# Optimization experiments

Measured on AMD Instinct MI355X. Metric: run time of the kernel, lower is better.

## Reference

```python
import jax, jax.numpy as jnp
import numpy as np

K_NEIGHBOURS = 40  # includes self; self is dropped after top-k


def setup_inputs() -> dict:
    key = jax.random.key(0)
    ks = jax.random.split(key, 4)
    B, V, F_in = 4, 4096, 64
    P, S, F_out = 64, 4, 64
    x = jax.random.normal(ks[0], (B, V, F_in), dtype=jnp.float32)
    Wf = jax.random.normal(ks[1], (F_in, P), dtype=jnp.float32) / np.sqrt(F_in)
    bf = jnp.zeros((P,), dtype=jnp.float32)
    Ws = jax.random.normal(ks[2], (F_in, S), dtype=jnp.float32) / np.sqrt(F_in)
    bs = jnp.zeros((S,), dtype=jnp.float32)
    Wo = jax.random.normal(ks[3], (F_in + 2 * P, F_out), dtype=jnp.float32) / np.sqrt(F_in + 2 * P)
    bo = jnpp = jnp.zeros((F_out,), dtype=jnp.float32)
    return {"x": x, "Wf": Wf, "bf": bf, "Ws": Ws, "bs": bs, "Wo": Wo, "bo": bo}


def _euclidean_squared(c):
    # c: [B, V, S] -> [B, V, V] squared pairwise distances
    sq = jnp.sum(c * c, axis=-1)  # [B, V]
    d2 = sq[:, :, None] + sq[:, None, :] - 2.0 * jnp.einsum('bvs,bus->bvu', c, c)
    return d2


def reference(x, Wf, bf, Ws, bs, Wo, bo):
    # learned spatial coordinates and propagated features
    coords = x @ Ws + bs            # [B, V, S]
    feats = x @ Wf + bf             # [B, V, P]

    d2 = _euclidean_squared(coords)                 # [B, V, V]
    neg_vals, idx = jax.lax.top_k(-d2, K_NEIGHBOURS)  # closest first (self at 0)
    nbr_idx = idx[:, :, 1:]                         # [B, V, K-1]
    dist = -neg_vals[:, :, 1:]                      # [B, V, K-1] (>= 0)

    # gauss_of_lin(d * 10) = exp(-|10 d|)
    w = jnp.exp(-jnp.abs(dist * 10.0))              # [B, V, K-1]

    # gather neighbour features per batch: [B, V, K-1, P]
    nf = jax.vmap(lambda f, i: f[i])(feats, nbr_idx)
    nf = nf * w[..., None]

    collected = jnp.concatenate([jnp.max(nf, axis=2), jnp.mean(nf, axis=2)], axis=-1)  # [B, V, 2P]
    updated = jnp.concatenate([x, collected], axis=-1)  # [B, V, F_in + 2P]
    return jnp.tanh(updated @ Wo + bo)
```

## Files before the change

### kernel.cpp

```cpp
#include <hip/hip_runtime.h>
#include <cmath>

#define BB  4
#define VV  4096
#define KK  40
#define FIN 64

typedef float v2f __attribute__((ext_vector_type(2)));

__global__ __launch_bounds__(256) void prep_kernel(
    const float* __restrict__ x, const float* __restrict__ Wf,
    const float* __restrict__ bf, const float* __restrict__ Ws,
    const float* __restrict__ bs,
    float* __restrict__ coords, float* __restrict__ sq,
    float* __restrict__ feats)
{
    int lane = threadIdx.x & 63;
    int wid  = threadIdx.x >> 6;
    int row0 = (blockIdx.x * 4 + wid) * 4;
    const float* xr = x + (size_t)row0 * FIN;

    float rx0 = xr[lane];
    float rx1 = xr[64  + lane];
    float rx2 = xr[128 + lane];
    float rx3 = xr[192 + lane];

    float a0 = 0.f, a1 = 0.f, a2 = 0.f, a3 = 0.f;
    #pragma unroll
    for (int k = 0; k < FIN; ++k) {
        float wf = Wf[k * 64 + lane];
        a0 = fmaf(__uint_as_float(
             __builtin_amdgcn_readlane(__float_as_uint(rx0), k)), wf, a0);
        a1 = fmaf(__uint_as_float(
             __builtin_amdgcn_readlane(__float_as_uint(rx1), k)), wf, a1);
        a2 = fmaf(__uint_as_float(
             __builtin_amdgcn_readlane(__float_as_uint(rx2), k)), wf, a2);
        a3 = fmaf(__uint_as_float(
             __builtin_amdgcn_readlane(__float_as_uint(rx3), k)), wf, a3);
    }
    float bfl = bf[lane];
    feats[(size_t)(row0 + 0) * 64 + lane] = a0 + bfl;
    feats[(size_t)(row0 + 1) * 64 + lane] = a1 + bfl;
    feats[(size_t)(row0 + 2) * 64 + lane] = a2 + bfl;
    feats[(size_t)(row0 + 3) * 64 + lane] = a3 + bfl;

    int r  = lane >> 4;
    int s  = (lane >> 2) & 3;
    int kc = lane & 3;
    const float* xrr = x + (size_t)(row0 + r) * FIN + kc * 16;
    const float* wsr = Ws + kc * 16 * 4 + s;
    float c = 0.f;
    #pragma unroll
    for (int k = 0; k < 16; ++k)
        c = fmaf(xrr[k], wsr[k * 4], c);
    c += __shfl_xor(c, 1, 64);
    c += __shfl_xor(c, 2, 64);
    float val = c + bs[s];
    if ((lane & 3) == 0) coords[(size_t)(row0 + r) * 4 + s] = val;
    float p = val * val;
    p += __shfl_xor(p, 4, 64);
    p += __shfl_xor(p, 8, 64);
    if ((lane & 15) == 0) sq[row0 + r] = p;
}

__device__ __forceinline__ unsigned umed3(unsigned a, unsigned b, unsigned c)
{
    unsigned d;
    asm("v_med3_u32 %0, %1, %2, %3" : "=v"(d) : "v"(a), "v"(b), "v"(c));
    return d;
}

__device__ __forceinline__ unsigned bfi_key(unsigned maskv, unsigned d2b,
                                            unsigned u)
{
    unsigned d;
    asm("v_bfi_b32 %0, %1, %2, %3" : "=v"(d) : "v"(maskv), "v"(d2b), "v"(u));
    return d;
}

__device__ __forceinline__ int cnt_lt4(unsigned m0, unsigned m1,
                                       unsigned m2, unsigned m3,
                                       unsigned cand)
{
    return (int)__popcll(__ballot(m0 < cand))
         + (int)__popcll(__ballot(m1 < cand))
         + (int)__popcll(__ballot(m2 < cand))
         + (int)__popcll(__ballot(m3 < cand));
}

__device__ __forceinline__ unsigned select_thresh(unsigned m0, unsigned m1,
                                                  unsigned m2, unsigned m3)
{
    unsigned M = 0u;
    #pragma unroll
    for (int bit = 30; bit >= 12; --bit) {
        unsigned cand = M | (1u << bit);
        if (cnt_lt4(m0, m1, m2, m3, cand) <= 39) M = cand;
    }
    unsigned Msel = M | 0xFFFu;
    if (cnt_lt4(m0, m1, m2, m3, M + 4096u) != 40) {
        #pragma unroll
        for (int bit = 11; bit >= 0; --bit) {
            unsigned cand = M | (1u << bit);
            if (cnt_lt4(m0, m1, m2, m3, cand) <= 39) M = cand;
        }
        Msel = M;
    }
    return Msel;
}

__device__ __forceinline__ void compact4(unsigned m0, unsigned m1,
                                         unsigned m2, unsigned m3,
                                         unsigned Msel, uint2* dst)
{
    unsigned mn = m0;
    #pragma unroll
    for (int off = 32; off >= 1; off >>= 1) {
        unsigned o = __shfl_xor(mn, off, 64);
        mn = o < mn ? o : mn;
    }
    int base = 0;
    unsigned kk = m0;
    #pragma unroll
    for (int i = 0; i < 4; ++i) {
        bool pred = (kk <= Msel) && (kk != mn);
        unsigned long long mask = __ballot(pred);
        unsigned pos = (unsigned)base +
            __builtin_amdgcn_mbcnt_hi((unsigned)(mask >> 32),
                __builtin_amdgcn_mbcnt_lo((unsigned)mask, 0u));
        if (pred) {
            float d2a = __uint_as_float(kk & 0xFFFFF000u);
            float w   = __expf(-10.f * d2a);
            dst[pos] = make_uint2((kk & 4095u) << 8, __float_as_uint(w));
        }
        base += (int)__popcll(mask);
        kk = (i == 0) ? m1 : (i == 1) ? m2 : m3;
    }
}

__global__ __launch_bounds__(128, 8) void gravnet_kernel(
    const float* __restrict__ x, const float* __restrict__ coords,
    const float* __restrict__ sq, const float* __restrict__ feats,
    const float* __restrict__ Wo, const float* __restrict__ bo,
    float* __restrict__ out)
{
    int lane = threadIdx.x & 63;
    int w    = threadIdx.x >> 6;
    int bid  = (int)((blockIdx.x & 7) * 512 + (blockIdx.x >> 3));
    int gw   = bid * 2 + w;
    int qb   = gw * 2;
    int b    = qb >> 12;
    int v0   = qb & (VV - 1);

    __shared__ __align__(16) char smem[4096];
    uint2* s_nb  = (uint2*)(smem + w * 2048);
    float* s_upd = (float*)(smem + w * 2048);

    const float4* cb  = (const float4*)(coords + (size_t)b * VV * 4);
    const float*  sqb = sq + (size_t)b * VV;

    float4 cq0 = cb[v0], cq1 = cb[v0 + 1];
    v2f nxA = (v2f){-2.f * cq0.x, -2.f * cq1.x};
    v2f nyA = (v2f){-2.f * cq0.y, -2.f * cq1.y};
    v2f nzA = (v2f){-2.f * cq0.z, -2.f * cq1.z};
    v2f nwA = (v2f){-2.f * cq0.w, -2.f * cq1.w};
    v2f hsA = (v2f){sqb[v0], sqb[v0 + 1]};

    unsigned k00 = ~0u, k01 = ~0u, k02 = ~0u, k03 = ~0u;
    unsigned k10 = ~0u, k11 = ~0u, k12 = ~0u, k13 = ~0u;

    unsigned maskv = 0xFFFFF000u;

    #pragma unroll 8
    for (int i = 0; i < 64; ++i) {
        int u = i * 64 + lane;
        float4 cu = cb[u];
        float squ = sqb[u];
        v2f accA = hsA + (v2f){squ, squ};
        accA = __builtin_elementwise_fma(nxA, (v2f){cu.x, cu.x}, accA);
        accA = __builtin_elementwise_fma(nyA, (v2f){cu.y, cu.y}, accA);
        accA = __builtin_elementwise_fma(nzA, (v2f){cu.z, cu.z}, accA);
        accA = __builtin_elementwise_fma(nwA, (v2f){cu.w, cu.w}, accA);

        {
            float d2 = fmaxf(accA.x, 0.f);
            unsigned k = bfi_key(maskv, __float_as_uint(d2), (unsigned)u);
            unsigned n1 = umed3(k00, k01, k);
            unsigned n2 = umed3(k01, k02, k);
            unsigned n3 = umed3(k02, k03, k);
            k00 = min(k00, k); k01 = n1; k02 = n2; k03 = n3;
        }
        {
            float d2 = fmaxf(accA.y, 0.f);
            unsigned k = bfi_key(maskv, __float_as_uint(d2), (unsigned)u);
            unsigned n1 = umed3(k10, k11, k);
            unsigned n2 = umed3(k11, k12, k);
            unsigned n3 = umed3(k12, k13, k);
            k10 = min(k10, k); k11 = n1; k12 = n2; k13 = n3;
        }
    }

    compact4(k00, k01, k02, k03,
             select_thresh(k00, k01, k02, k03), &s_nb[0]);
    compact4(k10, k11, k12, k13,
             select_thresh(k10, k11, k12, k13), &s_nb[KK]);

    const float* fb  = feats + (size_t)b * VV * 64;
    const char*  fbl = (const char*)(fb + lane);
    const uint4* nb0 = (const uint4*)&s_nb[0];
    const uint4* nb1 = (const uint4*)&s_nb[KK];
    v2f vmax01 = (v2f){-INFINITY, -INFINITY};
    v2f vsum01 = (v2f){0.f, 0.f};
    #pragma unroll 4
    for (int jp = 0; jp < 19; ++jp) {
        uint4 a = nb0[jp];
        uint4 c = nb1[jp];
        float f0a = *(const float*)(fbl + a.x);
        float f1a = *(const float*)(fbl + c.x);
        float f0b = *(const float*)(fbl + a.z);
        float f1b = *(const float*)(fbl + c.z);
        v2f ga = (v2f){f0a, f1a} *
                 (v2f){__uint_as_float(a.y), __uint_as_float(c.y)};
        v2f gb = (v2f){f0b, f1b} *
                 (v2f){__uint_as_float(a.w), __uint_as_float(c.w)};
        vmax01 = __builtin_elementwise_max(vmax01,
                 __builtin_elementwise_max(ga, gb));
        vsum01 += ga + gb;
    }
    {
        uint2 n0 = s_nb[38];
        uint2 n1 = s_nb[KK + 38];
        float f0 = *(const float*)(fbl + n0.x);
        float f1 = *(const float*)(fbl + n1.x);
        v2f g01 = (v2f){f0, f1} *
                  (v2f){__uint_as_float(n0.y), __uint_as_float(n1.y)};
        vmax01 = __builtin_elementwise_max(vmax01, g01);
        vsum01 += g01;
    }

    int q0g = qb, q1g = qb + 1;
    float* sb = s_upd;
    *(float2*)&sb[lane * 2] =
        make_float2(x[(size_t)q0g * 64 + lane], x[(size_t)q1g * 64 + lane]);
    *(float2*)&sb[128 + lane * 2] = make_float2(vmax01.x, vmax01.y);
    *(float2*)&sb[256 + lane * 2] =
        make_float2(vsum01.x * (1.0f / 39.0f), vsum01.y * (1.0f / 39.0f));

    float bol = bo[lane];
    v2f acc01 = (v2f){bol, bol};
    #pragma unroll 8
    for (int jj = 0; jj < 96; ++jj) {
        float wo0 = Wo[(jj * 2 + 0) * 64 + lane];
        float wo1 = Wo[(jj * 2 + 1) * 64 + lane];
        float4 up = *(const float4*)&sb[jj * 4];
        acc01 = __builtin_elementwise_fma((v2f){up.x, up.y},
                                          (v2f){wo0, wo0}, acc01);
        acc01 = __builtin_elementwise_fma((v2f){up.z, up.w},
                                          (v2f){wo1, wo1}, acc01);
    }
    float e0t = __expf(2.f * acc01.x);
    float e1t = __expf(2.f * acc01.y);
    out[(size_t)q0g * 64 + lane] = 1.f - __fdividef(2.f, e0t + 1.f);
    out[(size_t)q1g * 64 + lane] = 1.f - __fdividef(2.f, e1t + 1.f);
}

extern "C" void kernel_launch(void* const* d_in, const int* in_sizes, int n_in,
                              void* d_out, int out_size, void* d_ws, size_t ws_size,
                              hipStream_t stream)
{
    (void)in_sizes; (void)n_in; (void)out_size; (void)ws_size;
    const float* x  = (const float*)d_in[0];
    const float* Wf = (const float*)d_in[1];
    const float* bf = (const float*)d_in[2];
    const float* Ws = (const float*)d_in[3];
    const float* bs = (const float*)d_in[4];
    const float* Wo = (const float*)d_in[5];
    const float* bo = (const float*)d_in[6];
    float* out = (float*)d_out;

    float* coords = (float*)d_ws;
    float* sq     = coords + (size_t)BB * VV * 4;
    float* feats  = sq + (size_t)BB * VV;

    prep_kernel<<<BB * VV / 16, 256, 0, stream>>>(x, Wf, bf, Ws, bs,
                                                  coords, sq, feats);
    gravnet_kernel<<<BB * VV / 4, 128, 0, stream>>>(x, coords, sq, feats,
                                                    Wo, bo, out);
}
```

Before: 126.9 us.

## Process four queries per wave and four waves per block in gravnet kernel

Each wavefront now handles four query points instead of two. Every loaded candidate coordinate and every Wo row is reused across four queries, which halves global and L2 traffic per query for the distance scan and the output projection. Blocks grow from 128 to 256 threads with a matching grid and LDS size, and the launch bounds change to (256,4). The cost is more registers for the extra top-k state and accumulators, which may lower occupancy, and the grid has half as many waves, which reduces latency hiding.

```diff
diff --git a/kernel.cpp b/kernel.cpp
--- a/kernel.cpp
+++ b/kernel.cpp
@@ -138,7 +138,7 @@
     }
 }
 
-__global__ __launch_bounds__(128, 8) void gravnet_kernel(
+__global__ __launch_bounds__(256, 4) void gravnet_kernel(
     const float* __restrict__ x, const float* __restrict__ coords,
     const float* __restrict__ sq, const float* __restrict__ feats,
     const float* __restrict__ Wo, const float* __restrict__ bo,
@@ -146,32 +146,40 @@
 {
     int lane = threadIdx.x & 63;
     int w    = threadIdx.x >> 6;
-    int bid  = (int)((blockIdx.x & 7) * 512 + (blockIdx.x >> 3));
-    int gw   = bid * 2 + w;
-    int qb   = gw * 2;
+    int bid  = (int)((blockIdx.x & 7) * 128 + (blockIdx.x >> 3));
+    int gw   = bid * 4 + w;
+    int qb   = gw * 4;
     int b    = qb >> 12;
     int v0   = qb & (VV - 1);
 
-    __shared__ __align__(16) char smem[4096];
-    uint2* s_nb  = (uint2*)(smem + w * 2048);
-    float* s_upd = (float*)(smem + w * 2048);
+    __shared__ __align__(16) char smem[12288];
+    uint2* s_nb  = (uint2*)(smem + w * 3072);
+    float* s_upd = (float*)(smem + w * 3072);
 
     const float4* cb  = (const float4*)(coords + (size_t)b * VV * 4);
     const float*  sqb = sq + (size_t)b * VV;
 
-    float4 cq0 = cb[v0], cq1 = cb[v0 + 1];
+    float4 cq0 = cb[v0],     cq1 = cb[v0 + 1];
+    float4 cq2 = cb[v0 + 2], cq3 = cb[v0 + 3];
     v2f nxA = (v2f){-2.f * cq0.x, -2.f * cq1.x};
     v2f nyA = (v2f){-2.f * cq0.y, -2.f * cq1.y};
     v2f nzA = (v2f){-2.f * cq0.z, -2.f * cq1.z};
     v2f nwA = (v2f){-2.f * cq0.w, -2.f * cq1.w};
     v2f hsA = (v2f){sqb[v0], sqb[v0 + 1]};
+    v2f nxB = (v2f){-2.f * cq2.x, -2.f * cq3.x};
+    v2f nyB = (v2f){-2.f * cq2.y, -2.f * cq3.y};
+    v2f nzB = (v2f){-2.f * cq2.z, -2.f * cq3.z};
+    v2f nwB = (v2f){-2.f * cq2.w, -2.f * cq3.w};
+    v2f hsB = (v2f){sqb[v0 + 2], sqb[v0 + 3]};
 
     unsigned k00 = ~0u, k01 = ~0u, k02 = ~0u, k03 = ~0u;
     unsigned k10 = ~0u, k11 = ~0u, k12 = ~0u, k13 = ~0u;
+    unsigned k20 = ~0u, k21 = ~0u, k22 = ~0u, k23 = ~0u;
+    unsigned k30 = ~0u, k31 = ~0u, k32 = ~0u, k33 = ~0u;
 
     unsigned maskv = 0xFFFFF000u;
 
-    #pragma unroll 8
+    #pragma unroll 4
     for (int i = 0; i < 64; ++i) {
         int u = i * 64 + lane;
         float4 cu = cb[u];
@@ -181,6 +189,11 @@
         accA = __builtin_elementwise_fma(nyA, (v2f){cu.y, cu.y}, accA);
         accA = __builtin_elementwise_fma(nzA, (v2f){cu.z, cu.z}, accA);
         accA = __builtin_elementwise_fma(nwA, (v2f){cu.w, cu.w}, accA);
+        v2f accB = hsB + (v2f){squ, squ};
+        accB = __builtin_elementwise_fma(nxB, (v2f){cu.x, cu.x}, accB);
+        accB = __builtin_elementwise_fma(nyB, (v2f){cu.y, cu.y}, accB);
+        accB = __builtin_elementwise_fma(nzB, (v2f){cu.z, cu.z}, accB);
+        accB = __builtin_elementwise_fma(nwB, (v2f){cu.w, cu.w}, accB);
 
         {
             float d2 = fmaxf(accA.x, 0.f);
@@ -198,70 +211,122 @@
             unsigned n3 = umed3(k12, k13, k);
             k10 = min(k10, k); k11 = n1; k12 = n2; k13 = n3;
         }
+        {
+            float d2 = fmaxf(accB.x, 0.f);
+            unsigned k = bfi_key(maskv, __float_as_uint(d2), (unsigned)u);
+            unsigned n1 = umed3(k20, k21, k);
+            unsigned n2 = umed3(k21, k22, k);
+            unsigned n3 = umed3(k22, k23, k);
+            k20 = min(k20, k); k21 = n1; k22 = n2; k23 = n3;
+        }
+        {
+            float d2 = fmaxf(accB.y, 0.f);
+            unsigned k = bfi_key(maskv, __float_as_uint(d2), (unsigned)u);
+            unsigned n1 = umed3(k30, k31, k);
+            unsigned n2 = umed3(k31, k32, k);
+            unsigned n3 = umed3(k32, k33, k);
+            k30 = min(k30, k); k31 = n1; k32 = n2; k33 = n3;
+        }
     }
 
     compact4(k00, k01, k02, k03,
-             select_thresh(k00, k01, k02, k03), &s_nb[0]);
+             select_thresh(k00, k01, k02, k03), &s_nb[0 * KK]);
     compact4(k10, k11, k12, k13,
-             select_thresh(k10, k11, k12, k13), &s_nb[KK]);
+             select_thresh(k10, k11, k12, k13), &s_nb[1 * KK]);
+    compact4(k20, k21, k22, k23,
+             select_thresh(k20, k21, k22, k23), &s_nb[2 * KK]);
+    compact4(k30, k31, k32, k33,
+             select_thresh(k30, k31, k32, k33), &s_nb[3 * KK]);
 
     const float* fb  = feats + (size_t)b * VV * 64;
     const char*  fbl = (const char*)(fb + lane);
-    const uint4* nb0 = (const uint4*)&s_nb[0];
-    const uint4* nb1 = (const uint4*)&s_nb[KK];
+    const uint4* nb0 = (const uint4*)&s_nb[0 * KK];
+    const uint4* nb1 = (const uint4*)&s_nb[1 * KK];
+    const uint4* nb2 = (const uint4*)&s_nb[2 * KK];
+    const uint4* nb3 = (const uint4*)&s_nb[3 * KK];
     v2f vmax01 = (v2f){-INFINITY, -INFINITY};
     v2f vsum01 = (v2f){0.f, 0.f};
-    #pragma unroll 4
+    v2f vmax23 = (v2f){-INFINITY, -INFINITY};
+    v2f vsum23 = (v2f){0.f, 0.f};
+    #pragma unroll 2
     for (int jp = 0; jp < 19; ++jp) {
         uint4 a = nb0[jp];
         uint4 c = nb1[jp];
+        uint4 e = nb2[jp];
+        uint4 g = nb3[jp];
         float f0a = *(const float*)(fbl + a.x);
         float f1a = *(const float*)(fbl + c.x);
+        float f2a = *(const float*)(fbl + e.x);
+        float f3a = *(const float*)(fbl + g.x);
         float f0b = *(const float*)(fbl + a.z);
         float f1b = *(const float*)(fbl + c.z);
-        v2f ga = (v2f){f0a, f1a} *
-                 (v2f){__uint_as_float(a.y), __uint_as_float(c.y)};
-        v2f gb = (v2f){f0b, f1b} *
-                 (v2f){__uint_as_float(a.w), __uint_as_float(c.w)};
+        float f2b = *(const float*)(fbl + e.z);
+        float f3b = *(const float*)(fbl + g.z);
+        v2f ga01 = (v2f){f0a, f1a} *
+                   (v2f){__uint_as_float(a.y), __uint_as_float(c.y)};
+        v2f gb01 = (v2f){f0b, f1b} *
+                   (v2f){__uint_as_float(a.w), __uint_as_float(c.w)};
+        v2f ga23 = (v2f){f2a, f3a} *
+                   (v2f){__uint_as_float(e.y), __uint_as_float(g.y)};
+        v2f gb23 = (v2f){f2b, f3b} *
+                   (v2f){__uint_as_float(e.w), __uint_as_float(g.w)};
         vmax01 = __builtin_elementwise_max(vmax01,
-                 __builtin_elementwise_max(ga, gb));
-        vsum01 += ga + gb;
+                 __builtin_elementwise_max(ga01, gb01));
+        vsum01 += ga01 + gb01;
+        vmax23 = __builtin_elementwise_max(vmax23,
+                 __builtin_elementwise_max(ga23, gb23));
+        vsum23 += ga23 + gb23;
     }
     {
-        uint2 n0 = s_nb[38];
-        uint2 n1 = s_nb[KK + 38];
+        uint2 n0 = s_nb[0 * KK + 38];
+        uint2 n1 = s_nb[1 * KK + 38];
+        uint2 n2 = s_nb[2 * KK + 38];
+        uint2 n3 = s_nb[3 * KK + 38];
         float f0 = *(const float*)(fbl + n0.x);
         float f1 = *(const float*)(fbl + n1.x);
+        float f2 = *(const float*)(fbl + n2.x);
+        float f3 = *(const float*)(fbl + n3.x);
         v2f g01 = (v2f){f0, f1} *
                   (v2f){__uint_as_float(n0.y), __uint_as_float(n1.y)};
+        v2f g23 = (v2f){f2, f3} *
+                  (v2f){__uint_as_float(n2.y), __uint_as_float(n3.y)};
         vmax01 = __builtin_elementwise_max(vmax01, g01);
         vsum01 += g01;
-    }
-
-    int q0g = qb, q1g = qb + 1;
+        vmax23 = __builtin_elementwise_max(vmax23, g23);
+        vsum23 += g23;
+    }
+
+    int q0g = qb, q1g = qb + 1, q2g = qb + 2, q3g = qb + 3;
     float* sb = s_upd;
-    *(float2*)&sb[lane * 2] =
-        make_float2(x[(size_t)q0g * 64 + lane], x[(size_t)q1g * 64 + lane]);
-    *(float2*)&sb[128 + lane * 2] = make_float2(vmax01.x, vmax01.y);
-    *(float2*)&sb[256 + lane * 2] =
-        make_float2(vsum01.x * (1.0f / 39.0f), vsum01.y * (1.0f / 39.0f));
+    *(float4*)&sb[lane * 4] =
+        make_float4(x[(size_t)q0g * 64 + lane], x[(size_t)q1g * 64 + lane],
+                    x[(size_t)q2g * 64 + lane], x[(size_t)q3g * 64 + lane]);
+    *(float4*)&sb[256 + lane * 4] =
+        make_float4(vmax01.x, vmax01.y, vmax23.x, vmax23.y);
+    *(float4*)&sb[512 + lane * 4] =
+        make_float4(vsum01.x * (1.0f / 39.0f), vsum01.y * (1.0f / 39.0f),
+                    vsum23.x * (1.0f / 39.0f), vsum23.y * (1.0f / 39.0f));
 
     float bol = bo[lane];
     v2f acc01 = (v2f){bol, bol};
+    v2f acc23 = (v2f){bol, bol};
     #pragma unroll 8
-    for (int jj = 0; jj < 96; ++jj) {
-        float wo0 = Wo[(jj * 2 + 0) * 64 + lane];
-        float wo1 = Wo[(jj * 2 + 1) * 64 + lane];
-        float4 up = *(const float4*)&sb[jj * 4];
+    for (int j = 0; j < 192; ++j) {
+        float wo = Wo[j * 64 + lane];
+        float4 up = *(const float4*)&sb[j * 4];
         acc01 = __builtin_elementwise_fma((v2f){up.x, up.y},
-                                          (v2f){wo0, wo0}, acc01);
-        acc01 = __builtin_elementwise_fma((v2f){up.z, up.w},
-                                          (v2f){wo1, wo1}, acc01);
+                                          (v2f){wo, wo}, acc01);
+        acc23 = __builtin_elementwise_fma((v2f){up.z, up.w},
+                                          (v2f){wo, wo}, acc23);
     }
     float e0t = __expf(2.f * acc01.x);
     float e1t = __expf(2.f * acc01.y);
+    float e2t = __expf(2.f * acc23.x);
+    float e3t = __expf(2.f * acc23.y);
     out[(size_t)q0g * 64 + lane] = 1.f - __fdividef(2.f, e0t + 1.f);
     out[(size_t)q1g * 64 + lane] = 1.f - __fdividef(2.f, e1t + 1.f);
+    out[(size_t)q2g * 64 + lane] = 1.f - __fdividef(2.f, e2t + 1.f);
+    out[(size_t)q3g * 64 + lane] = 1.f - __fdividef(2.f, e3t + 1.f);
 }
 
 extern "C" void kernel_launch(void* const* d_in, const int* in_sizes, int n_in,
@@ -284,6 +349,6 @@
 
     prep_kernel<<<BB * VV / 16, 256, 0, stream>>>(x, Wf, bf, Ws, bs,
                                                   coords, sq, feats);
-    gravnet_kernel<<<BB * VV / 4, 128, 0, stream>>>(x, coords, sq, feats,
-                                                    Wo, bo, out);
-}
+    gravnet_kernel<<<BB * VV / 16, 256, 0, stream>>>(x, coords, sq, feats,
+                                                     Wo, bo, out);
+}
```

After: 118.8 us. -6.4%, faster.
